# Kernel optimization log

Hardware: AMD Instinct MI355X
Metric: run time of the kernel (lower is better)

## Reference

```python
import jax, jax.numpy as jnp
import numpy as np

NUM_HEADS = 16
LN_EPS = 1e-5

def _layernorm(x, g, b):
    m = jnp.mean(x, axis=-1, keepdims=True)
    v = jnp.var(x, axis=-1, keepdims=True)
    return (x - m) * jax.lax.rsqrt(v + LN_EPS) * g + b

def _mha(xq, xkv, qw, qb, kw, kb, vw, vb, ow, ob, causal):
    B, T, D = xq.shape
    S = xkv.shape[1]
    Hd = D // NUM_HEADS
    q = (xq @ qw + qb).reshape(B, T, NUM_HEADS, Hd)
    k = (xkv @ kw + kb).reshape(B, S, NUM_HEADS, Hd)
    v = (xkv @ vw + vb).reshape(B, S, NUM_HEADS, Hd)
    scores = jnp.einsum('bthd,bshd->bhts', q, k) / np.sqrt(Hd).astype(np.float32)
    if causal:
        mask = jnp.arange(T)[:, None] >= jnp.arange(S)[None, :]
        scores = jnp.where(mask, scores, jnp.float32(-jnp.inf))
    attn = jax.nn.softmax(scores, axis=-1)
    out = jnp.einsum('bhts,bshd->bthd', attn, v).reshape(B, T, D)
    return out @ ow + ob

def setup_inputs() -> dict:
    B, T, S, D, F = 4, 2048, 2048, 1024, 4096
    key = jax.random.key(0)
    ks = jax.random.split(key, 16)
    w = lambda k, shape: jax.random.normal(k, shape, dtype=jnp.float32) * 0.02
    z = lambda n: jnp.zeros((n,), jnp.float32)
    o = lambda n: jnp.ones((n,), jnp.float32)
    return {
        'x': jax.random.normal(ks[0], (B, T, D), dtype=jnp.float32),
        'encoder_output': jax.random.normal(ks[1], (B, S, D), dtype=jnp.float32),
        'sa_qw': w(ks[2], (D, D)), 'sa_qb': z(D),
        'sa_kw': w(ks[3], (D, D)), 'sa_kb': z(D),
        'sa_vw': w(ks[4], (D, D)), 'sa_vb': z(D),
        'sa_ow': w(ks[5], (D, D)), 'sa_ob': z(D),
        'ca_qw': w(ks[6], (D, D)), 'ca_qb': z(D),
        'ca_kw': w(ks[7], (D, D)), 'ca_kb': z(D),
        'ca_vw': w(ks[8], (D, D)), 'ca_vb': z(D),
        'ca_ow': w(ks[9], (D, D)), 'ca_ob': z(D),
        'ff_w1': w(ks[10], (D, F)), 'ff_b1': z(F),
        'ff_w2': w(ks[11], (F, D)), 'ff_b2': z(D),
        'ln1_g': o(D), 'ln1_b': z(D),
        'ln2_g': o(D), 'ln2_b': z(D),
        'ln3_g': o(D), 'ln3_b': z(D),
    }

def reference(x, encoder_output,
              sa_qw, sa_qb, sa_kw, sa_kb, sa_vw, sa_vb, sa_ow, sa_ob,
              ca_qw, ca_qb, ca_kw, ca_kb, ca_vw, ca_vb, ca_ow, ca_ob,
              ff_w1, ff_b1, ff_w2, ff_b2,
              ln1_g, ln1_b, ln2_g, ln2_b, ln3_g, ln3_b):
    # pre-norm causal self-attn + residual
    h = _layernorm(x, ln1_g, ln1_b)
    x = x + _mha(h, h, sa_qw, sa_qb, sa_kw, sa_kb, sa_vw, sa_vb, sa_ow, sa_ob, causal=True)
    # pre-norm cross-attn + residual
    h = _layernorm(x, ln2_g, ln2_b)
    x = x + _mha(h, encoder_output, ca_qw, ca_qb, ca_kw, ca_kb, ca_vw, ca_vb, ca_ow, ca_ob, causal=False)
    # pre-norm FFN + residual (dropout = identity in eval)
    h = _layernorm(x, ln3_g, ln3_b)
    x = x + (jax.nn.relu(h @ ff_w1 + ff_b1) @ ff_w2 + ff_b2)
    return x
```

## Files before the change

### kernel.cpp

```cpp
#include <hip/hip_runtime.h>
#include <stdint.h>

#define D_MODEL 1024
#define D_FF    4096
#define NHEADS  16
#define HD      64
#define LN_EPS  1e-5f

using u16 = unsigned short;
typedef __bf16 bf16x8 __attribute__((ext_vector_type(8)));
typedef float  f32x4  __attribute__((ext_vector_type(4)));
typedef float  f32x16 __attribute__((ext_vector_type(16)));

typedef __attribute__((address_space(1))) uint32_t as1_u32;
typedef __attribute__((address_space(3))) uint32_t as3_u32;

__device__ __forceinline__ u16 f2bf(float f) {
  union { float f; uint32_t u; } v; v.f = f;
  uint32_t r = v.u + 0x7FFFu + ((v.u >> 16) & 1u);
  return (u16)(r >> 16);
}

__device__ __forceinline__ float bf2f(u16 u) {
  union { uint32_t u; float f; } v; v.u = (uint32_t)u << 16; return v.f;
}

__device__ __forceinline__ uint32_t cvtpk(float lo, float hi) {
  uint32_t r;
  asm("v_cvt_pk_bf16_f32 %0, %1, %2" : "=v"(r) : "v"(lo), "v"(hi));
  return r;
}

__device__ __forceinline__ void gl_lds16(const void* g, void* l) {
  __builtin_amdgcn_global_load_lds((const as1_u32*)(uintptr_t)g,
                                   (as3_u32*)(uint32_t)(uintptr_t)l, 16, 0, 0);
}

__global__ __launch_bounds__(256)
void transpose_cast(const float* __restrict__ W, u16* __restrict__ Wt, int K, int N) {
  __shared__ float t[32][33];
  const int k0 = blockIdx.x * 32, n0 = blockIdx.y * 32;
  const int x = threadIdx.x & 31, y = threadIdx.x >> 5;
#pragma unroll
  for (int j = 0; j < 32; j += 8)
    t[y + j][x] = W[(size_t)(k0 + y + j) * N + (n0 + x)];
  __syncthreads();
#pragma unroll
  for (int j = 0; j < 32; j += 8)
    Wt[(size_t)(n0 + y + j) * K + (k0 + x)] = f2bf(t[x][y + j]);
}

struct Src8 { const float* s[8]; };
__global__ __launch_bounds__(256)
void transpose_cast8(Src8 p, u16* __restrict__ dstbase) {
  __shared__ float t[32][33];
  const float* __restrict__ W = p.s[blockIdx.z];
  u16* __restrict__ Wt = dstbase + (size_t)blockIdx.z * (1024 * 1024);
  const int k0 = blockIdx.x * 32, n0 = blockIdx.y * 32;
  const int x = threadIdx.x & 31, y = threadIdx.x >> 5;
#pragma unroll
  for (int j = 0; j < 32; j += 8)
    t[y + j][x] = W[(size_t)(k0 + y + j) * 1024 + (n0 + x)];
  __syncthreads();
#pragma unroll
  for (int j = 0; j < 32; j += 8)
    Wt[(size_t)(n0 + y + j) * 1024 + (k0 + x)] = f2bf(t[x][y + j]);
}

__global__ __launch_bounds__(256)
void cast_f32_bf16(const float* __restrict__ in, u16* __restrict__ out, int n4) {
  int i = blockIdx.x * 256 + threadIdx.x;
  if (i < n4) {
    float4 v = ((const float4*)in)[i];
    ushort4 o;
    o.x = f2bf(v.x); o.y = f2bf(v.y); o.z = f2bf(v.z); o.w = f2bf(v.w);
    ((ushort4*)out)[i] = o;
  }
}

template<int BF16IN>
__global__ __launch_bounds__(256)
void ln_bf16(const float* __restrict__ xf, const u16* __restrict__ xb,
             const float* __restrict__ g, const float* __restrict__ bta,
             u16* __restrict__ out) {
  const int row = blockIdx.x;
  const int tid = threadIdx.x;
  float4 v;
  if (BF16IN) {
    ushort4 u = ((const ushort4*)(xb + (size_t)row * D_MODEL))[tid];
    v.x = bf2f(u.x); v.y = bf2f(u.y); v.z = bf2f(u.z); v.w = bf2f(u.w);
  } else {
    v = ((const float4*)(xf + (size_t)row * D_MODEL))[tid];
  }
  float s  = v.x + v.y + v.z + v.w;
  float s2 = v.x * v.x + v.y * v.y + v.z * v.z + v.w * v.w;
#pragma unroll
  for (int off = 1; off < 64; off <<= 1) {
    s  += __shfl_xor(s, off);
    s2 += __shfl_xor(s2, off);
  }
  __shared__ float sm[8];
  const int wave = tid >> 6, lane = tid & 63;
  if (lane == 0) { sm[wave] = s; sm[4 + wave] = s2; }
  __syncthreads();
  s  = sm[0] + sm[1] + sm[2] + sm[3];
  s2 = sm[4] + sm[5] + sm[6] + sm[7];
  const float mean = s * (1.f / D_MODEL);
  const float var  = s2 * (1.f / D_MODEL) - mean * mean;
  const float rstd = rsqrtf(var + LN_EPS);
  const float4 gv = ((const float4*)g)[tid];
  const float4 bv = ((const float4*)bta)[tid];
  ushort4 o;
  o.x = f2bf((v.x - mean) * rstd * gv.x + bv.x);
  o.y = f2bf((v.y - mean) * rstd * gv.y + bv.y);
  o.z = f2bf((v.z - mean) * rstd * gv.z + bv.z);
  o.w = f2bf((v.w - mean) * rstd * gv.w + bv.w);
  ((ushort4*)(out + (size_t)row * D_MODEL))[tid] = o;
}

#define QSCALE 0.18033688011112042f
template<int EPI>
__global__ __launch_bounds__(256, 3)
void gemm_bf16(const u16* __restrict__ A, const u16* __restrict__ Wt,
               const float* __restrict__ bias, const float* __restrict__ bias2,
               const float* __restrict__ bias3,
               const float* __restrict__ residf, const u16* __restrict__ residb,
               u16* __restrict__ outb, u16* __restrict__ outb2, u16* __restrict__ outb3,
               float* outf, int M, int N, int K) {
  __shared__ u16 lA[128 * 32];
  __shared__ u16 lB[128 * 32];
  const int tid  = threadIdx.x;
  const int lane = tid & 63;
  const int wave = tid >> 6;
  const int wr = wave >> 1, wc = wave & 1;
  const int lr = lane & 15, lg = lane >> 4;
  const int row0 = blockIdx.x * 128, col0 = blockIdx.y * 128;

  const char* pa = (const char*)A  + ((size_t)(row0 + (tid >> 2)) * K + (size_t)(tid & 3) * 8) * 2;
  const char* pb = (const char*)Wt + ((size_t)(col0 + (tid >> 2)) * K + (size_t)(tid & 3) * 8) * 2;
  const size_t rowskip = (size_t)64 * K * 2;
  char* la = (char*)lA + wave * 1024;
  char* lb = (char*)lB + wave * 1024;

  f32x4 acc[4][4] = {};
  const int ksteps = K >> 5;
  for (int kt = 0; kt < ksteps; ++kt) {
    gl_lds16(pa, la);
    gl_lds16(pa + rowskip, la + 4096);
    gl_lds16(pb, lb);
    gl_lds16(pb + rowskip, lb + 4096);
    pa += 64; pb += 64;
    __syncthreads();
    bf16x8 af[4], bfr[4];
#pragma unroll
    for (int m = 0; m < 4; ++m)
      af[m] = *(const bf16x8*)((const char*)lA + (wr * 64 + m * 16 + lr) * 64 + lg * 16);
#pragma unroll
    for (int n = 0; n < 4; ++n)
      bfr[n] = *(const bf16x8*)((const char*)lB + (wc * 64 + n * 16 + lr) * 64 + lg * 16);
#pragma unroll
    for (int m = 0; m < 4; ++m)
#pragma unroll
      for (int n = 0; n < 4; ++n)
        acc[m][n] = __builtin_amdgcn_mfma_f32_16x16x32_bf16(af[m], bfr[n], acc[m][n], 0, 0, 0);
    __syncthreads();
  }

#pragma unroll
  for (int m = 0; m < 4; ++m) {
    const int grow = row0 + wr * 64 + m * 16 + lg * 4;
#pragma unroll
    for (int n = 0; n < 4; ++n) {
      const int gcol = col0 + wc * 64 + n * 16 + lr;
      if (EPI == 4 || EPI == 5) {
        const int seg = gcol >> 10;
        const int c = gcol & 1023;
        float bv;
        float sc = 1.f;
        u16* optr;
        if (EPI == 4) {
          bv = ((seg == 0) ? bias : (seg == 1) ? bias2 : bias3)[c];
          optr = (seg == 0) ? outb : (seg == 1) ? outb2 : outb3;
          if (seg == 0) sc = QSCALE;
        } else {
          bv = (seg ? bias2 : bias)[c];
          optr = seg ? outb2 : outb;
        }
#pragma unroll
        for (int r = 0; r < 4; ++r)
          optr[(size_t)(grow + r) * 1024 + c] = f2bf((acc[m][n][r] + bv) * sc);
      } else {
        const float bv = bias[gcol];
#pragma unroll
        for (int r = 0; r < 4; ++r) {
          const size_t idx = (size_t)(grow + r) * N + gcol;
          float v = acc[m][n][r] + bv;
          if (EPI == 0)      outb[idx] = f2bf(v);
          else if (EPI == 1) outb[idx] = f2bf(v > 0.f ? v : 0.f);
          else if (EPI == 2) outb[idx] = f2bf(v + residf[idx]);
          else if (EPI == 3) outb[idx] = f2bf(v * QSCALE);
          else if (EPI == 6) outb[idx] = f2bf(v + bf2f(residb[idx]));
          else               outf[idx] = v + bf2f(residb[idx]);
        }
      }
    }
  }
}

template<bool CAUSAL>
__global__ __launch_bounds__(256, 4)
void attn_kernel(const u16* __restrict__ Q, const u16* __restrict__ Kb,
                 const u16* __restrict__ Vb, u16* __restrict__ O,
                 int T, int S) {
  __shared__ u16 lQ[128 * 64];
  __shared__ u16 lK[64 * 64];
  __shared__ u16 lVt[64 * 64];

  const int f  = blockIdx.x;
  const int bh = f & 63;
  const int b = bh >> 4, hd = bh & 15;
  const int qx = f >> 6;
  const int q0 = (CAUSAL ? (T / 128 - 1 - qx) : qx) * 128;
  const int tid = threadIdx.x, lane = tid & 63, wave = tid >> 6;
  const int l31 = lane & 31, hb = lane >> 5;

  const u16* Qbase = Q  + (size_t)(b * T) * D_MODEL + hd * HD;
  const u16* Kbase = Kb + (size_t)(b * S) * D_MODEL + hd * HD;
  const u16* Vbase = Vb + (size_t)(b * S) * D_MODEL + hd * HD;
  const size_t rskip = (size_t)32 * D_MODEL * 2;

  const int srow = tid >> 3;
  const int sg   = (tid & 7) ^ (srow & 7);
  const int sprow = (srow & ~12) | ((srow & 4) << 1) | ((srow & 8) >> 1);

  {
    const char* src = (const char*)(Qbase + (size_t)(q0 + srow) * D_MODEL) + sg * 16;
    char* dst = (char*)lQ + wave * 1024;
    gl_lds16(src,             dst);
    gl_lds16(src + rskip,     dst + 4096);
    gl_lds16(src + 2 * rskip, dst + 8192);
    gl_lds16(src + 3 * rskip, dst + 12288);
  }

  bf16x8 qf[4];
  f32x16 oacc0 = {}, oacc1 = {};
  float m_run = -1e30f, l_run = 0.f;
  const int qq = q0 + wave * 32 + l31;

  const int ktEnd = CAUSAL ? (q0 / 64 + 2) : (S / 64);

  for (int kt = 0; kt < ktEnd; ++kt) {
    {
      const char* src = (const char*)(Kbase + (size_t)(kt * 64 + sprow) * D_MODEL) + sg * 16;
      char* dst = (char*)lK + wave * 1024;
      gl_lds16(src, dst);
      gl_lds16(src + rskip, dst + 4096);
    }
    {
      const u16* src = Vbase + (size_t)(kt * 64 + (tid >> 3)) * D_MODEL + (tid & 7) * 8;
      union { uint4 q; u16 s[8]; } v0, v1;
      v0.q = *(const uint4*)src;
      v1.q = *(const uint4*)(src + 32 * D_MODEL);
      const int key = tid >> 3, dbase = (tid & 7) * 8;
      const int kg0 = key >> 3, kb0 = (key & 7) * 2;
      const int kg1 = kg0 + 4;
#pragma unroll
      for (int j = 0; j < 8; ++j) {
        const int d = dbase + j;
        const int sw = (d >> 3) & 7;
        char* base = (char*)lVt + d * 128;
        *(u16*)(base + ((kg0 ^ sw) << 4) + kb0) = v0.s[j];
        *(u16*)(base + ((kg1 ^ sw) << 4) + kb0) = v1.s[j];
      }
    }
    __syncthreads();

    if (kt == 0) {
      const int qrow = wave * 32 + l31;
#pragma unroll
      for (int dc = 0; dc < 4; ++dc)
        qf[dc] = *(const bf16x8*)((const char*)lQ + qrow * 128 +
                                  (((2 * dc + hb) ^ (qrow & 7)) << 4));
    }

    const bool live = !CAUSAL || (kt * 64 <= q0 + wave * 32 + 31);
    if (live) {
      f32x16 z0 = {}, z1 = {};
      __builtin_amdgcn_s_setprio(1);
#pragma unroll
      for (int dc = 0; dc < 4; ++dc) {
        bf16x8 kf0 = *(const bf16x8*)((const char*)lK + l31 * 128 +
                                      (((2 * dc + hb) ^ (l31 & 7)) << 4));
        z0 = __builtin_amdgcn_mfma_f32_32x32x16_bf16(kf0, qf[dc], z0, 0, 0, 0);
      }
#pragma unroll
      for (int dc = 0; dc < 4; ++dc) {
        bf16x8 kf1 = *(const bf16x8*)((const char*)lK + (32 + l31) * 128 +
                                      (((2 * dc + hb) ^ (l31 & 7)) << 4));
        z1 = __builtin_amdgcn_mfma_f32_32x32x16_bf16(kf1, qf[dc], z1, 0, 0, 0);
      }
      __builtin_amdgcn_s_setprio(0);

      if (CAUSAL && kt * 64 + 63 > q0 + wave * 32) {
        const int kvb = kt * 64 + 8 * hb;
#pragma unroll
        for (int r = 0; r < 16; ++r) {
          const int kv = kvb + (r & 7) + 16 * (r >> 3);
          if (kv > qq)      z0[r] = -1e30f;
          if (kv + 32 > qq) z1[r] = -1e30f;
        }
      }

      float t[16];
#pragma unroll
      for (int r = 0; r < 16; ++r) t[r] = fmaxf(z0[r], z1[r]);
#pragma unroll
      for (int sdt = 8; sdt >= 1; sdt >>= 1)
#pragma unroll
        for (int i = 0; i < 8; ++i)
          if (i < sdt) t[i] = fmaxf(t[i], t[i + sdt]);
      float mx = t[0];
      mx = fmaxf(mx, __shfl_xor(mx, 32));

      if (!__all(mx - m_run <= 11.5f)) {
        const float mn = fmaxf(m_run, mx);
        const float scl = exp2f(m_run - mn);
        m_run = mn;
        l_run *= scl;
#pragma unroll
        for (int r = 0; r < 16; ++r) { oacc0[r] *= scl; oacc1[r] *= scl; }
      }
      float sum = 0.f;
#pragma unroll
      for (int r = 0; r < 16; ++r) {
        z0[r] = exp2f(z0[r] - m_run); sum += z0[r];
        z1[r] = exp2f(z1[r] - m_run); sum += z1[r];
      }
      sum += __shfl_xor(sum, 32);
      l_run += sum;

      bf16x8 pf[4];
      {
        union { uint32_t u[4]; bf16x8 v; } w0, w1, w2, w3;
#pragma unroll
        for (int i = 0; i < 4; ++i) {
          w0.u[i] = cvtpk(z0[2 * i],     z0[2 * i + 1]);
          w1.u[i] = cvtpk(z0[8 + 2 * i], z0[9 + 2 * i]);
          w2.u[i] = cvtpk(z1[2 * i],     z1[2 * i + 1]);
          w3.u[i] = cvtpk(z1[8 + 2 * i], z1[9 + 2 * i]);
        }
        pf[0] = w0.v; pf[1] = w1.v; pf[2] = w2.v; pf[3] = w3.v;
      }

      __builtin_amdgcn_s_setprio(1);
#pragma unroll
      for (int c = 0; c < 4; ++c) {
        bf16x8 vf0 = *(const bf16x8*)((const char*)lVt + l31 * 128 +
                       (((2 * c + hb) ^ ((l31 >> 3) & 7)) << 4));
        oacc0 = __builtin_amdgcn_mfma_f32_32x32x16_bf16(vf0, pf[c], oacc0, 0, 0, 0);
        bf16x8 vf1 = *(const bf16x8*)((const char*)lVt + (32 + l31) * 128 +
                       ((((2 * c + hb) ^ (((32 + l31) >> 3) & 7))) << 4));
        oacc1 = __builtin_amdgcn_mfma_f32_32x32x16_bf16(vf1, pf[c], oacc1, 0, 0, 0);
      }
      __builtin_amdgcn_s_setprio(0);
    }
    __syncthreads();
  }

  const float linv = 1.f / l_run;
  u16* Op = O + (size_t)(b * T + qq) * D_MODEL + hd * HD + 4 * hb;
#pragma unroll
  for (int rr = 0; rr < 4; ++rr) {
    uint2 st0, st1;
    st0.x = cvtpk(oacc0[4 * rr + 0] * linv, oacc0[4 * rr + 1] * linv);
    st0.y = cvtpk(oacc0[4 * rr + 2] * linv, oacc0[4 * rr + 3] * linv);
    *(uint2*)(Op + 8 * rr) = st0;
    st1.x = cvtpk(oacc1[4 * rr + 0] * linv, oacc1[4 * rr + 1] * linv);
    st1.y = cvtpk(oacc1[4 * rr + 2] * linv, oacc1[4 * rr + 3] * linv);
    *(uint2*)(Op + 32 + 8 * rr) = st1;
  }
}

extern "C" void kernel_launch(void* const* d_in, const int* in_sizes, int n_in,
                              void* d_out, int out_size, void* d_ws, size_t ws_size,
                              hipStream_t stream) {
  (void)in_sizes; (void)n_in; (void)out_size; (void)ws_size;
  const int B = 4, T = 2048, S = 2048, Dm = 1024, F = 4096;
  const int M = B * T;

  const float* x   = (const float*)d_in[0];
  const float* enc = (const float*)d_in[1];

  char* p = (char*)d_ws;
  auto take = [&](size_t bytes) { char* r = p; p += (bytes + 255) & ~(size_t)255; return r; };
  u16* wt8  = (u16*)take((size_t)8 * Dm * Dm * 2);
  u16* ff1T = (u16*)take((size_t)F * Dm * 2);
  u16* ff2T = (u16*)take((size_t)Dm * F * 2);
  u16*   h    = (u16*)take((size_t)M * Dm * 2);
  u16*   encb = (u16*)take((size_t)M * Dm * 2);
  u16*   xc   = (u16*)take((size_t)M * Dm * 2);
  u16*   xc2  = (u16*)take((size_t)M * Dm * 2);
  char*  Dreg = take((size_t)M * F * 2);
  u16* qb = (u16*)Dreg;
  u16* kb = (u16*)(Dreg + (size_t)M * Dm * 2);
  u16* vb = (u16*)(Dreg + (size_t)2 * M * Dm * 2);
  u16* ab = (u16*)(Dreg + (size_t)3 * M * Dm * 2);
  u16* ffmid = (u16*)Dreg;

  dim3 blk(256);
  Src8 s8 = {{ (const float*)d_in[2], (const float*)d_in[4], (const float*)d_in[6],
               (const float*)d_in[8], (const float*)d_in[10], (const float*)d_in[12],
               (const float*)d_in[14], (const float*)d_in[16] }};
  transpose_cast8<<<dim3(32, 32, 8), blk, 0, stream>>>(s8, wt8);
  transpose_cast<<<dim3(Dm / 32, F / 32), blk, 0, stream>>>((const float*)d_in[18], ff1T, Dm, F);
  transpose_cast<<<dim3(F / 32, Dm / 32), blk, 0, stream>>>((const float*)d_in[20], ff2T, F, Dm);
  cast_f32_bf16<<<dim3((M * Dm / 4) / 256), blk, 0, stream>>>(enc, encb, M * Dm / 4);

  dim3 gproj(M / 128, Dm / 128);
  dim3 gqkv(M / 128, 3072 / 128);
  dim3 gkv(M / 128, 2048 / 128);
  dim3 gffn1(M / 128, F / 128);
  dim3 gattn((T / 128) * 64);

  ln_bf16<0><<<M, blk, 0, stream>>>(x, nullptr, (const float*)d_in[22], (const float*)d_in[23], h);
  gemm_bf16<4><<<gqkv, blk, 0, stream>>>(h, wt8,
      (const float*)d_in[3], (const float*)d_in[5], (const float*)d_in[7],
      nullptr, nullptr, qb, kb, vb, nullptr, M, 3072, Dm);
  attn_kernel<true><<<gattn, blk, 0, stream>>>(qb, kb, vb, ab, T, S);
  gemm_bf16<2><<<gproj, blk, 0, stream>>>(ab, wt8 + (size_t)3 * Dm * Dm,
      (const float*)d_in[9], nullptr, nullptr, x, nullptr, xc, nullptr, nullptr, nullptr, M, Dm, Dm);

  ln_bf16<1><<<M, blk, 0, stream>>>(nullptr, xc, (const float*)d_in[24], (const float*)d_in[25], h);
  gemm_bf16<3><<<gproj, blk, 0, stream>>>(h, wt8 + (size_t)4 * Dm * Dm,
      (const float*)d_in[11], nullptr, nullptr, nullptr, nullptr, qb, nullptr, nullptr, nullptr, M, Dm, Dm);
  gemm_bf16<5><<<gkv, blk, 0, stream>>>(encb, wt8 + (size_t)5 * Dm * Dm,
      (const float*)d_in[13], (const float*)d_in[15], nullptr,
      nullptr, nullptr, kb, vb, nullptr, nullptr, M, 2048, Dm);
  attn_kernel<false><<<gattn, blk, 0, stream>>>(qb, kb, vb, ab, T, S);
  gemm_bf16<6><<<gproj, blk, 0, stream>>>(ab, wt8 + (size_t)7 * Dm * Dm,
      (const float*)d_in[17], nullptr, nullptr, nullptr, xc, xc2, nullptr, nullptr, nullptr, M, Dm, Dm);

  ln_bf16<1><<<M, blk, 0, stream>>>(nullptr, xc2, (const float*)d_in[26], (const float*)d_in[27], h);
  gemm_bf16<1><<<gffn1, blk, 0, stream>>>(h, ff1T, (const float*)d_in[19],
      nullptr, nullptr, nullptr, nullptr, ffmid, nullptr, nullptr, nullptr, M, F, Dm);
  gemm_bf16<7><<<gproj, blk, 0, stream>>>(ffmid, ff2T, (const float*)d_in[21],
      nullptr, nullptr, nullptr, xc2, nullptr, nullptr, nullptr, (float*)d_out, M, Dm, F);
}
```

Baseline: 605.2 us.

## Double GEMM K-tile to 64 and XOR-swizzle LDS layout

The bf16 GEMM now stages a 128x64 K-slice of A and W per iteration instead of 128x32, which halves the number of barrier pairs per K. Global-to-LDS loads are remapped to 8 threads per row, and the 16-byte chunk index is XOR-swizzled by row so the MFMA fragment reads avoid LDS bank conflicts. LDS use per block doubles to 32 KB, which may limit how many blocks fit per CU under the launch bound of 3.

```diff
diff --git a/kernel.cpp b/kernel.cpp
--- a/kernel.cpp
+++ b/kernel.cpp
@@ -127,8 +127,8 @@
                const float* __restrict__ residf, const u16* __restrict__ residb,
                u16* __restrict__ outb, u16* __restrict__ outb2, u16* __restrict__ outb3,
                float* outf, int M, int N, int K) {
-  __shared__ u16 lA[128 * 32];
-  __shared__ u16 lB[128 * 32];
+  __shared__ u16 lA[128 * 64];
+  __shared__ u16 lB[128 * 64];
   const int tid  = threadIdx.x;
   const int lane = tid & 63;
   const int wave = tid >> 6;
@@ -136,33 +136,48 @@
   const int lr = lane & 15, lg = lane >> 4;
   const int row0 = blockIdx.x * 128, col0 = blockIdx.y * 128;
 
-  const char* pa = (const char*)A  + ((size_t)(row0 + (tid >> 2)) * K + (size_t)(tid & 3) * 8) * 2;
-  const char* pb = (const char*)Wt + ((size_t)(col0 + (tid >> 2)) * K + (size_t)(tid & 3) * 8) * 2;
-  const size_t rowskip = (size_t)64 * K * 2;
+  const int srow8 = tid >> 3;
+  const int sg    = (tid & 7) ^ (srow8 & 7);
+  const char* pa = (const char*)A  + ((size_t)(row0 + srow8) * K) * 2 + sg * 16;
+  const char* pb = (const char*)Wt + ((size_t)(col0 + srow8) * K) * 2 + sg * 16;
+  const size_t cskip = (size_t)32 * K * 2;
   char* la = (char*)lA + wave * 1024;
   char* lb = (char*)lB + wave * 1024;
 
   f32x4 acc[4][4] = {};
-  const int ksteps = K >> 5;
+  const int ksteps = K >> 6;
   for (int kt = 0; kt < ksteps; ++kt) {
-    gl_lds16(pa, la);
-    gl_lds16(pa + rowskip, la + 4096);
-    gl_lds16(pb, lb);
-    gl_lds16(pb + rowskip, lb + 4096);
-    pa += 64; pb += 64;
+    gl_lds16(pa,             la);
+    gl_lds16(pa + cskip,     la + 4096);
+    gl_lds16(pa + 2 * cskip, la + 8192);
+    gl_lds16(pa + 3 * cskip, la + 12288);
+    gl_lds16(pb,             lb);
+    gl_lds16(pb + cskip,     lb + 4096);
+    gl_lds16(pb + 2 * cskip, lb + 8192);
+    gl_lds16(pb + 3 * cskip, lb + 12288);
+    pa += 128; pb += 128;
     __syncthreads();
-    bf16x8 af[4], bfr[4];
-#pragma unroll
-    for (int m = 0; m < 4; ++m)
-      af[m] = *(const bf16x8*)((const char*)lA + (wr * 64 + m * 16 + lr) * 64 + lg * 16);
-#pragma unroll
-    for (int n = 0; n < 4; ++n)
-      bfr[n] = *(const bf16x8*)((const char*)lB + (wc * 64 + n * 16 + lr) * 64 + lg * 16);
-#pragma unroll
-    for (int m = 0; m < 4; ++m)
-#pragma unroll
-      for (int n = 0; n < 4; ++n)
-        acc[m][n] = __builtin_amdgcn_mfma_f32_16x16x32_bf16(af[m], bfr[n], acc[m][n], 0, 0, 0);
+#pragma unroll
+    for (int kk = 0; kk < 2; ++kk) {
+      bf16x8 af[4], bfr[4];
+#pragma unroll
+      for (int m = 0; m < 4; ++m) {
+        const int rr = wr * 64 + m * 16 + lr;
+        af[m] = *(const bf16x8*)((const char*)lA + rr * 128 +
+                                 (((kk * 4 + lg) ^ (rr & 7)) << 4));
+      }
+#pragma unroll
+      for (int n = 0; n < 4; ++n) {
+        const int rr = wc * 64 + n * 16 + lr;
+        bfr[n] = *(const bf16x8*)((const char*)lB + rr * 128 +
+                                  (((kk * 4 + lg) ^ (rr & 7)) << 4));
+      }
+#pragma unroll
+      for (int m = 0; m < 4; ++m)
+#pragma unroll
+        for (int n = 0; n < 4; ++n)
+          acc[m][n] = __builtin_amdgcn_mfma_f32_16x16x32_bf16(af[m], bfr[n], acc[m][n], 0, 0, 0);
+    }
     __syncthreads();
   }
 
```

Measured after the change: 563.4 us (median of 2 runs). -6.9%, faster.
